# Performance work log

Hardware: AMD Instinct MI355X
Metric: run time of the kernel (lower is better)

Reference implementation:

```python
import jax, jax.numpy as jnp
import numpy as np

TAU = 0.07
MIN_PIXELS = 3
LAMBDA_CF = 0.5
NUM_INST = 16  # labels in patch_mask are 0 (bg) .. NUM_INST
N, D = 65536, 256


def _l2norm(x, axis=-1):
    n = jnp.linalg.norm(x, axis=axis, keepdims=True)
    return x / jnp.maximum(n, 1e-12)


def setup_inputs() -> dict:
    key = jax.random.key(0)
    k1, k2, k3 = jax.random.split(key, 3)
    dp = jax.random.normal(k1, (N, D), dtype=jnp.float32)
    f_cf = jax.random.normal(k2, (N, D), dtype=jnp.float32)
    patch_mask = jax.random.randint(k3, (N,), 0, NUM_INST + 1, dtype=jnp.int32)
    return {"dp": dp, "f_cf": f_cf, "patch_mask": patch_mask}


def reference(dp, f_cf, patch_mask):
    K1 = NUM_INST + 1  # segment 0 = background, 1..K = instances
    labels = patch_mask
    dpn = _l2norm(dp)       # [N, D]
    cfn = _l2norm(f_cf)     # [N, D]

    ones = jnp.ones((labels.shape[0],), dtype=dp.dtype)
    cnt = jax.ops.segment_sum(ones, labels, num_segments=K1)         # [K1]
    sum_dp = jax.ops.segment_sum(dpn, labels, num_segments=K1)       # [K1, D]
    sum_cf = jax.ops.segment_sum(cfn, labels, num_segments=K1)       # [K1, D]
    safe_cnt = jnp.maximum(cnt, 1.0)

    mu_dp = _l2norm(sum_dp / safe_cnt[:, None])   # per-segment normalized mean of dp
    mu_cf = _l2norm(sum_cf / safe_cnt[:, None])   # per-segment normalized mean of f_cf
    mu_bg_dp = mu_dp[0]                           # [D]
    mu_bg_cf = mu_cf[0]                           # [D]

    # per-pixel similarities
    pos_t = jnp.sum(dpn * mu_dp[labels], axis=-1)      # dp . mu_{k(label)}
    neg_t = dpn @ mu_bg_dp                             # dp . mu_bg
    # -log(exp(p/tau)/(exp(p/tau)+exp(n/tau))) == softplus((n-p)/tau)
    pix_loss_t = jax.nn.softplus((neg_t - pos_t) / TAU)

    pos_cf = cfn @ mu_bg_cf                            # f_cf . mu_bg_cf (the 'pos' in the cf term)
    oth_cf = jnp.sum(cfn * mu_cf[labels], axis=-1)     # f_cf . mu_k_cf
    pix_loss_cf = jax.nn.softplus((oth_cf - pos_cf) / TAU)

    seg_loss_t = jax.ops.segment_sum(pix_loss_t, labels, num_segments=K1) / safe_cnt
    seg_loss_cf = jax.ops.segment_sum(pix_loss_cf, labels, num_segments=K1) / safe_cnt

    inst_ids = jnp.arange(K1)
    valid = (inst_ids > 0) & (cnt >= MIN_PIXELS)       # instances with enough pixels
    n_valid = jnp.maximum(jnp.sum(valid.astype(dp.dtype)), 1.0)

    loss_t = jnp.sum(jnp.where(valid, seg_loss_t, 0.0)) / n_valid
    loss_cf = jnp.sum(jnp.where(valid, seg_loss_cf, 0.0)) / n_valid
    return loss_t + LAMBDA_CF * loss_cf
```

## Files before the change

kernel.cpp:

```cpp
#include <hip/hip_runtime.h>
#include <math.h>

#define K1 17
#define SEG_F (K1 * 256)
#define PART_F (2 * SEG_F + 32)
#define NGRP 8

#define SCALE_SUM 65536.0f
#define INV_SUM   (1.0f / 65536.0f)
#define SCALE_L   8192.0f
#define INV_L     (1.0f / 8192.0f)

#define GRED_BASE 0
#define MU_BASE   (NGRP * 2 * SEG_F)
#define GCNT_OFF  (MU_BASE + 2 * SEG_F)
#define LT_OFF    (GCNT_OFF + K1)
#define LC_OFF    (LT_OFF + K1)
#define PART_BASE 78400

template <int CTRL, int RMASK>
__device__ __forceinline__ float dpp_add(float x) {
    int t = __builtin_amdgcn_update_dpp(0, __float_as_int(x), CTRL, RMASK, 0xf, false);
    return x + __int_as_float(t);
}
__device__ __forceinline__ float wave_sum_nb(float x) {
    x = dpp_add<0x111, 0xf>(x);
    x = dpp_add<0x112, 0xf>(x);
    x = dpp_add<0x114, 0xf>(x);
    x = dpp_add<0x118, 0xf>(x);
    x = dpp_add<0x142, 0xa>(x);
    x = dpp_add<0x143, 0xc>(x);
    return x;
}
__device__ __forceinline__ float wave_sum(float x) {
    return __int_as_float(__builtin_amdgcn_readlane(__float_as_int(wave_sum_nb(x)), 63));
}
__device__ __forceinline__ float dot4s(const float4 v) {
    return v.x * v.x + v.y * v.y + v.z * v.z + v.w * v.w;
}
__device__ __forceinline__ float softplus_f(float x) {
    const float a = -fabsf(x) * 1.4426950408889634f;
    float e; asm("v_exp_f32 %0, %1" : "=v"(e) : "v"(a));
    float l; asm("v_log_f32 %0, %1" : "=v"(l) : "v"(1.0f + e));
    return fmaxf(x, 0.0f) + l * 0.6931471805599453f;
}
__device__ __forceinline__ float rsq_f(float x) {
    float r; asm("v_rsq_f32 %0, %1" : "=v"(r) : "v"(x));
    return r;
}

__device__ __forceinline__ void kA_commit(int* __restrict__ s, const float4 v, const float4 w,
                                          float nd, float nc, int l, int lane)
{
    const float f = SCALE_SUM * rsq_f(fmaxf(nd, 1e-24f));
    const float g = SCALE_SUM * rsq_f(fmaxf(nc, 1e-24f));
    int* a = s + l * 256 + lane;
    atomicAdd(a,       (int)(v.x * f));
    atomicAdd(a + 64,  (int)(v.y * f));
    atomicAdd(a + 128, (int)(v.z * f));
    atomicAdd(a + 192, (int)(v.w * f));
    int* b = a + SEG_F;
    atomicAdd(b,       (int)(w.x * g));
    atomicAdd(b + 64,  (int)(w.y * g));
    atomicAdd(b + 128, (int)(w.z * g));
    atomicAdd(b + 192, (int)(w.w * g));
}

__global__ __launch_bounds__(1024) void kA(const float4* __restrict__ dp, const float4* __restrict__ cf,
                                           const int* __restrict__ mask, float* __restrict__ part,
                                           int nPart, int nRows)
{
    __shared__ int s[2 * SEG_F];
    __shared__ int hist[K1];
    const int tid = threadIdx.x;
    for (int i = tid; i < 2 * SEG_F; i += 1024) s[i] = 0;
    if (tid < K1) hist[tid] = 0;
    __syncthreads();

    const int lane = tid & 63;
    const int wid = tid >> 6;
    const int rpb = (nRows + nPart - 1) / nPart;
    const int base = blockIdx.x * rpb;
    const int end = (base + rpb < nRows) ? base + rpb : nRows;

    int r = base + wid;
    for (; r + 16 < end; r += 32) {
        const int l0 = mask[r], l1 = mask[r + 16];
        const float4 v0 = dp[(size_t)r * 64 + lane];
        const float4 w0 = cf[(size_t)r * 64 + lane];
        const float4 v1 = dp[(size_t)(r + 16) * 64 + lane];
        const float4 w1 = cf[(size_t)(r + 16) * 64 + lane];
        const float nd0 = wave_sum(dot4s(v0));
        const float nc0 = wave_sum(dot4s(w0));
        const float nd1 = wave_sum(dot4s(v1));
        const float nc1 = wave_sum(dot4s(w1));
        kA_commit(s, v0, w0, nd0, nc0, l0, lane);
        kA_commit(s, v1, w1, nd1, nc1, l1, lane);
        if (lane == 0) { atomicAdd(&hist[l0], 1); atomicAdd(&hist[l1], 1); }
    }
    for (; r < end; r += 16) {
        const int l0 = mask[r];
        const float4 v0 = dp[(size_t)r * 64 + lane];
        const float4 w0 = cf[(size_t)r * 64 + lane];
        const float nd0 = wave_sum(dot4s(v0));
        const float nc0 = wave_sum(dot4s(w0));
        kA_commit(s, v0, w0, nd0, nc0, l0, lane);
        if (lane == 0) atomicAdd(&hist[l0], 1);
    }
    __syncthreads();
    float* outp = part + (size_t)blockIdx.x * PART_F;
    for (int i = tid; i < 2 * SEG_F; i += 1024) outp[i] = (float)s[i] * INV_SUM;
    if (tid < K1) outp[2 * SEG_F + tid] = (float)hist[tid];
}

__global__ __launch_bounds__(256) void kRed(const float* __restrict__ part, float* __restrict__ gred, int nPart)
{
    const int col = blockIdx.x * 256 + threadIdx.x;
    const int g = blockIdx.y;
    const int per = nPart / NGRP;
    const float* p = part + (size_t)g * per * PART_F + col;
    float acc = 0.0f;
    for (int b = 0; b < per; ++b) acc += p[(size_t)b * PART_F];
    gred[g * (2 * SEG_F) + col] = acc;
}

__global__ __launch_bounds__(256) void k_mu(float* __restrict__ ws, int nPart)
{
    const int k = blockIdx.x, t = threadIdx.x;
    __shared__ float C[256];
    float c = 0.0f;
    for (int b = t; b < nPart; b += 256) c += ws[PART_BASE + (size_t)b * PART_F + 2 * SEG_F + k];
    C[t] = c; __syncthreads();
    for (int s2 = 128; s2 > 0; s2 >>= 1) { if (t < s2) C[t] += C[t + s2]; __syncthreads(); }
    const float cnt = C[0];
    const float safe = fmaxf(cnt, 1.0f);
    float sd = 0.0f, sc = 0.0f;
    #pragma unroll
    for (int g = 0; g < NGRP; ++g) {
        sd += ws[GRED_BASE + g * 2 * SEG_F + k * 256 + t];
        sc += ws[GRED_BASE + g * 2 * SEG_F + SEG_F + k * 256 + t];
    }
    const float md = sd / safe, mc = sc / safe;
    __shared__ float A[256], B[256];
    A[t] = md * md; B[t] = mc * mc;
    __syncthreads();
    for (int s2 = 128; s2 > 0; s2 >>= 1) { if (t < s2) { A[t] += A[t + s2]; B[t] += B[t + s2]; } __syncthreads(); }
    const float id = 1.0f / fmaxf(sqrtf(A[0]), 1e-12f);
    const float ic = 1.0f / fmaxf(sqrtf(B[0]), 1e-12f);
    const int dnat = 4 * (t & 63) + (t >> 6);
    ws[MU_BASE + k * 256 + dnat]         = md * id;
    ws[MU_BASE + SEG_F + k * 256 + dnat] = mc * ic;
    if (t == 0) ws[GCNT_OFF + k] = cnt;
}

__device__ __forceinline__ void row_part(const float4 v, const float4 w, int l, int lane,
                                         const float4* __restrict__ mud, const float4* __restrict__ muc,
                                         const float4 bd, const float4 bc,
                                         float& nd, float& nc, float& dd, float& dc)
{
    const float4 md = mud[l * 64 + lane];
    const float4 mc = muc[l * 64 + lane];
    nd = dot4s(v);
    nc = dot4s(w);
    dd = v.x * (bd.x - md.x) + v.y * (bd.y - md.y) + v.z * (bd.z - md.z) + v.w * (bd.w - md.w);
    dc = w.x * (mc.x - bc.x) + w.y * (mc.y - bc.y) + w.z * (mc.z - bc.z) + w.w * (mc.w - bc.w);
}
__device__ __forceinline__ void row_commit(float nd, float nc, float dd, float dc, int l, int tid63,
                                           int* __restrict__ lt, int* __restrict__ lc)
{
    const float invd = rsq_f(fmaxf(nd, 1e-24f));
    const float invc = rsq_f(fmaxf(nc, 1e-24f));
    const float xt = dd * invd * (1.0f / 0.07f);
    const float xc = dc * invc * (1.0f / 0.07f);
    const float plt = softplus_f(xt);
    const float plc = softplus_f(xc);
    if (tid63) {
        atomicAdd(&lt[l], (int)(plt * SCALE_L + 0.5f));
        atomicAdd(&lc[l], (int)(plc * SCALE_L + 0.5f));
    }
}

__global__ __launch_bounds__(512) void k_loss(const float4* __restrict__ dp, const float4* __restrict__ cf,
                                              const int* __restrict__ mask, float* __restrict__ ws,
                                              int nBlocks, int nRows)
{
    __shared__ float4 mud[SEG_F / 4], muc[SEG_F / 4];
    __shared__ int lt[K1], lc[K1];
    const int tid = threadIdx.x;
    const float4* musrc = (const float4*)(ws + MU_BASE);
    for (int i = tid; i < SEG_F / 4; i += 512) { mud[i] = musrc[i]; muc[i] = musrc[SEG_F / 4 + i]; }
    if (tid < K1) { lt[tid] = 0; lc[tid] = 0; }
    __syncthreads();

    const int lane = tid & 63;
    const int wid = tid >> 6;
    const int rpb = (nRows + nBlocks - 1) / nBlocks;
    const int base = blockIdx.x * rpb;
    const int end = (base + rpb < nRows) ? base + rpb : nRows;
    const int isl63 = (lane == 63);

    const float4 bd = mud[lane];
    const float4 bc = muc[lane];

    int r = base + wid;
    for (; r + 8 < end; r += 16) {
        const int l0 = mask[r], l1 = mask[r + 8];
        const float4 v0 = dp[(size_t)r * 64 + lane];
        const float4 w0 = cf[(size_t)r * 64 + lane];
        const float4 v1 = dp[(size_t)(r + 8) * 64 + lane];
        const float4 w1 = cf[(size_t)(r + 8) * 64 + lane];
        float nd0, nc0, dd0, dc0, nd1, nc1, dd1, dc1;
        row_part(v0, w0, l0, lane, mud, muc, bd, bc, nd0, nc0, dd0, dc0);
        row_part(v1, w1, l1, lane, mud, muc, bd, bc, nd1, nc1, dd1, dc1);
        nd0 = wave_sum_nb(nd0); nc0 = wave_sum_nb(nc0); dd0 = wave_sum_nb(dd0); dc0 = wave_sum_nb(dc0);
        nd1 = wave_sum_nb(nd1); nc1 = wave_sum_nb(nc1); dd1 = wave_sum_nb(dd1); dc1 = wave_sum_nb(dc1);
        row_commit(nd0, nc0, dd0, dc0, l0, isl63, lt, lc);
        row_commit(nd1, nc1, dd1, dc1, l1, isl63, lt, lc);
    }
    for (; r < end; r += 8) {
        const int l0 = mask[r];
        const float4 v0 = dp[(size_t)r * 64 + lane];
        const float4 w0 = cf[(size_t)r * 64 + lane];
        float nd0, nc0, dd0, dc0;
        row_part(v0, w0, l0, lane, mud, muc, bd, bc, nd0, nc0, dd0, dc0);
        nd0 = wave_sum_nb(nd0); nc0 = wave_sum_nb(nc0); dd0 = wave_sum_nb(dd0); dc0 = wave_sum_nb(dc0);
        row_commit(nd0, nc0, dd0, dc0, l0, isl63, lt, lc);
    }
    __syncthreads();
    if (tid < K1) {
        int* LT = (int*)ws + LT_OFF;
        int* LC = (int*)ws + LC_OFF;
        atomicAdd(&LT[tid], lt[tid]);
        atomicAdd(&LC[tid], lc[tid]);
    }
}

__global__ void k_final(const float* __restrict__ ws, float* __restrict__ out)
{
    const int t = threadIdx.x;
    const int* LT = (const int*)ws + LT_OFF;
    const int* LC = (const int*)ws + LC_OFF;
    float vt = 0.0f, vc = 0.0f, nv = 0.0f;
    if (t >= 1 && t < K1) {
        const float cnt = ws[GCNT_OFF + t];
        if (cnt >= 3.0f) {
            const float safe = fmaxf(cnt, 1.0f);
            vt = (float)LT[t] * INV_L / safe;
            vc = (float)LC[t] * INV_L / safe;
            nv = 1.0f;
        }
    }
    #pragma unroll
    for (int o = 32; o > 0; o >>= 1) {
        vt += __shfl_xor(vt, o, 64);
        vc += __shfl_xor(vc, o, 64);
        nv += __shfl_xor(nv, o, 64);
    }
    if (t == 0) {
        const float n = fmaxf(nv, 1.0f);
        out[0] = vt / n + 0.5f * (vc / n);
    }
}

extern "C" void kernel_launch(void* const* d_in, const int* in_sizes, int n_in,
                              void* d_out, int out_size, void* d_ws, size_t ws_size,
                              hipStream_t stream)
{
    const float4* dp = (const float4*)d_in[0];
    const float4* cf = (const float4*)d_in[1];
    const int* mask  = (const int*)d_in[2];
    float* ws  = (float*)d_ws;
    float* out = (float*)d_out;
    const int nRows = in_sizes[2];

    long availF = (long)(ws_size / 4) - PART_BASE;
    int nPart = (int)(availF / PART_F);
    if (nPart > 512) nPart = 512;
    nPart &= ~7;
    if (nPart < 8) nPart = 8;

    hipMemsetAsync((void*)(ws + LT_OFF), 0, 2 * K1 * sizeof(int), stream);
    kA<<<nPart, 1024, 0, stream>>>(dp, cf, mask, ws + PART_BASE, nPart, nRows);
    kRed<<<dim3(34, NGRP), 256, 0, stream>>>(ws + PART_BASE, ws + GRED_BASE, nPart);
    k_mu<<<K1, 256, 0, stream>>>(ws, nPart);
    const int nB3 = 1024;
    k_loss<<<nB3, 512, 0, stream>>>(dp, cf, mask, ws, nB3, nRows);
    k_final<<<1, 64, 0, stream>>>(ws, out);
}
```

Before: 97.69 us.

## Fuse final reduction into loss kernel via last-block counter, drop memset launch

Removes the separate k_final launch by having the last k_loss block, detected through an atomic done counter, compute the final scalar. The accumulator zeroing moves from a hipMemsetAsync into k_mu, removing another launch. The partial-block count in kA is also capped at 256 instead of 512, which gives kA fewer, larger blocks and leaves kRed less to reduce. In exchange it adds threadfences and a serial tail in one thread, and relies on the memory ordering of the completion counter.

```diff
diff --git a/kernel.cpp b/kernel.cpp
--- a/kernel.cpp
+++ b/kernel.cpp
@@ -16,6 +16,7 @@
 #define GCNT_OFF  (MU_BASE + 2 * SEG_F)
 #define LT_OFF    (GCNT_OFF + K1)
 #define LC_OFF    (LT_OFF + K1)
+#define DONE_OFF  (LC_OFF + K1)
 #define PART_BASE 78400
 
 template <int CTRL, int RMASK>
@@ -127,6 +128,7 @@
 __global__ __launch_bounds__(256) void k_mu(float* __restrict__ ws, int nPart)
 {
     const int k = blockIdx.x, t = threadIdx.x;
+    if (k == 0 && t < 2 * K1 + 1) ((int*)ws)[LT_OFF + t] = 0;
     __shared__ float C[256];
     float c = 0.0f;
     for (int b = t; b < nPart; b += 256) c += ws[PART_BASE + (size_t)b * PART_F + 2 * SEG_F + k];
@@ -182,7 +184,7 @@
 
 __global__ __launch_bounds__(512) void k_loss(const float4* __restrict__ dp, const float4* __restrict__ cf,
                                               const int* __restrict__ mask, float* __restrict__ ws,
-                                              int nBlocks, int nRows)
+                                              float* __restrict__ out, int nBlocks, int nRows)
 {
     __shared__ float4 mud[SEG_F / 4], muc[SEG_F / 4];
     __shared__ int lt[K1], lc[K1];
@@ -227,38 +229,31 @@
         row_commit(nd0, nc0, dd0, dc0, l0, isl63, lt, lc);
     }
     __syncthreads();
+    int* LT = (int*)ws + LT_OFF;
+    int* LC = (int*)ws + LC_OFF;
     if (tid < K1) {
-        int* LT = (int*)ws + LT_OFF;
-        int* LC = (int*)ws + LC_OFF;
         atomicAdd(&LT[tid], lt[tid]);
         atomicAdd(&LC[tid], lc[tid]);
     }
-}
-
-__global__ void k_final(const float* __restrict__ ws, float* __restrict__ out)
-{
-    const int t = threadIdx.x;
-    const int* LT = (const int*)ws + LT_OFF;
-    const int* LC = (const int*)ws + LC_OFF;
-    float vt = 0.0f, vc = 0.0f, nv = 0.0f;
-    if (t >= 1 && t < K1) {
-        const float cnt = ws[GCNT_OFF + t];
-        if (cnt >= 3.0f) {
-            const float safe = fmaxf(cnt, 1.0f);
-            vt = (float)LT[t] * INV_L / safe;
-            vc = (float)LC[t] * INV_L / safe;
-            nv = 1.0f;
+    __syncthreads();
+    if (tid == 0) {
+        __threadfence();
+        const int prev = atomicAdd((int*)ws + DONE_OFF, 1);
+        if (prev == nBlocks - 1) {
+            __threadfence();
+            float vt = 0.0f, vc = 0.0f, nv = 0.0f;
+            for (int k = 1; k < K1; ++k) {
+                const float cnt = ws[GCNT_OFF + k];
+                if (cnt >= 3.0f) {
+                    const float safe = fmaxf(cnt, 1.0f);
+                    vt += (float)atomicAdd(&LT[k], 0) * INV_L / safe;
+                    vc += (float)atomicAdd(&LC[k], 0) * INV_L / safe;
+                    nv += 1.0f;
+                }
+            }
+            const float n = fmaxf(nv, 1.0f);
+            out[0] = vt / n + 0.5f * (vc / n);
         }
-    }
-    #pragma unroll
-    for (int o = 32; o > 0; o >>= 1) {
-        vt += __shfl_xor(vt, o, 64);
-        vc += __shfl_xor(vc, o, 64);
-        nv += __shfl_xor(nv, o, 64);
-    }
-    if (t == 0) {
-        const float n = fmaxf(nv, 1.0f);
-        out[0] = vt / n + 0.5f * (vc / n);
     }
 }
 
@@ -275,15 +270,13 @@
 
     long availF = (long)(ws_size / 4) - PART_BASE;
     int nPart = (int)(availF / PART_F);
-    if (nPart > 512) nPart = 512;
+    if (nPart > 256) nPart = 256;
     nPart &= ~7;
     if (nPart < 8) nPart = 8;
 
-    hipMemsetAsync((void*)(ws + LT_OFF), 0, 2 * K1 * sizeof(int), stream);
     kA<<<nPart, 1024, 0, stream>>>(dp, cf, mask, ws + PART_BASE, nPart, nRows);
     kRed<<<dim3(34, NGRP), 256, 0, stream>>>(ws + PART_BASE, ws + GRED_BASE, nPart);
     k_mu<<<K1, 256, 0, stream>>>(ws, nPart);
     const int nB3 = 1024;
-    k_loss<<<nB3, 512, 0, stream>>>(dp, cf, mask, ws, nB3, nRows);
-    k_final<<<1, 64, 0, stream>>>(ws, out);
-}
+    k_loss<<<nB3, 512, 0, stream>>>(dp, cf, mask, ws, out, nB3, nRows);
+}
```

New measurement: 99.81 us. 1.02x slower.

## Cache normalized rows as FP8 in pass one and fold mu differences

Applied to the files above, without the earlier changes.

The first pass now also writes each row's L2-normalized dp and f_cf vectors as scaled FP8 into the workspace. The loss pass then reads these 1-byte copies instead of re-reading both fp32 inputs, and no longer recomputes row norms. k_mu now precomputes the difference between the background and segment mean vectors, so the loss pass needs one dot product per tensor. The memset is folded into k_mu and the partition count is fixed. The aim is to cut the second pass's HBM traffic, at the cost of FP8 quantization error in the per-pixel dots, which the softplus amplifies through the 1/tau scale.

```diff
diff --git a/kernel.cpp b/kernel.cpp
--- a/kernel.cpp
+++ b/kernel.cpp
@@ -5,11 +5,14 @@
 #define SEG_F (K1 * 256)
 #define PART_F (2 * SEG_F + 32)
 #define NGRP 8
+#define NPART 256
 
 #define SCALE_SUM 65536.0f
 #define INV_SUM   (1.0f / 65536.0f)
 #define SCALE_L   8192.0f
 #define INV_L     (1.0f / 8192.0f)
+#define FP8_SCALE 16.0f
+#define TAU_INV   (1.0f / 0.07f)
 
 #define GRED_BASE 0
 #define MU_BASE   (NGRP * 2 * SEG_F)
@@ -17,6 +20,9 @@
 #define LT_OFF    (GCNT_OFF + K1)
 #define LC_OFF    (LT_OFF + K1)
 #define PART_BASE 78400
+#define FP8D_BASE (PART_BASE + NPART * PART_F)
+
+typedef float v2f __attribute__((ext_vector_type(2)));
 
 template <int CTRL, int RMASK>
 __device__ __forceinline__ float dpp_add(float x) {
@@ -49,11 +55,15 @@
     return r;
 }
 
+template <bool W8>
 __device__ __forceinline__ void kA_commit(int* __restrict__ s, const float4 v, const float4 w,
-                                          float nd, float nc, int l, int lane)
-{
-    const float f = SCALE_SUM * rsq_f(fmaxf(nd, 1e-24f));
-    const float g = SCALE_SUM * rsq_f(fmaxf(nc, 1e-24f));
+                                          float nd, float nc, int l, int lane,
+                                          unsigned* __restrict__ q8d, unsigned* __restrict__ q8c)
+{
+    const float ir = rsq_f(fmaxf(nd, 1e-24f));
+    const float jr = rsq_f(fmaxf(nc, 1e-24f));
+    const float f = SCALE_SUM * ir;
+    const float g = SCALE_SUM * jr;
     int* a = s + l * 256 + lane;
     atomicAdd(a,       (int)(v.x * f));
     atomicAdd(a + 64,  (int)(v.y * f));
@@ -64,10 +74,22 @@
     atomicAdd(b + 64,  (int)(w.y * g));
     atomicAdd(b + 128, (int)(w.z * g));
     atomicAdd(b + 192, (int)(w.w * g));
-}
-
+    if (W8) {
+        const float fe = FP8_SCALE * ir;
+        const float ge = FP8_SCALE * jr;
+        int pd = __builtin_amdgcn_cvt_pk_fp8_f32(v.x * fe, v.y * fe, 0, false);
+        pd     = __builtin_amdgcn_cvt_pk_fp8_f32(v.z * fe, v.w * fe, pd, true);
+        int pc = __builtin_amdgcn_cvt_pk_fp8_f32(w.x * ge, w.y * ge, 0, false);
+        pc     = __builtin_amdgcn_cvt_pk_fp8_f32(w.z * ge, w.w * ge, pc, true);
+        *q8d = (unsigned)pd;
+        *q8c = (unsigned)pc;
+    }
+}
+
+template <bool W8>
 __global__ __launch_bounds__(1024) void kA(const float4* __restrict__ dp, const float4* __restrict__ cf,
                                            const int* __restrict__ mask, float* __restrict__ part,
+                                           unsigned* __restrict__ qd, unsigned* __restrict__ qc,
                                            int nPart, int nRows)
 {
     __shared__ int s[2 * SEG_F];
@@ -94,8 +116,8 @@
         const float nc0 = wave_sum(dot4s(w0));
         const float nd1 = wave_sum(dot4s(v1));
         const float nc1 = wave_sum(dot4s(w1));
-        kA_commit(s, v0, w0, nd0, nc0, l0, lane);
-        kA_commit(s, v1, w1, nd1, nc1, l1, lane);
+        kA_commit<W8>(s, v0, w0, nd0, nc0, l0, lane, qd + (size_t)r * 64 + lane,        qc + (size_t)r * 64 + lane);
+        kA_commit<W8>(s, v1, w1, nd1, nc1, l1, lane, qd + (size_t)(r + 16) * 64 + lane, qc + (size_t)(r + 16) * 64 + lane);
         if (lane == 0) { atomicAdd(&hist[l0], 1); atomicAdd(&hist[l1], 1); }
     }
     for (; r < end; r += 16) {
@@ -104,7 +126,7 @@
         const float4 w0 = cf[(size_t)r * 64 + lane];
         const float nd0 = wave_sum(dot4s(v0));
         const float nc0 = wave_sum(dot4s(w0));
-        kA_commit(s, v0, w0, nd0, nc0, l0, lane);
+        kA_commit<W8>(s, v0, w0, nd0, nc0, l0, lane, qd + (size_t)r * 64 + lane, qc + (size_t)r * 64 + lane);
         if (lane == 0) atomicAdd(&hist[l0], 1);
     }
     __syncthreads();
@@ -127,68 +149,69 @@
 __global__ __launch_bounds__(256) void k_mu(float* __restrict__ ws, int nPart)
 {
     const int k = blockIdx.x, t = threadIdx.x;
+    if (k == 0 && t < 2 * K1) ((int*)ws)[LT_OFF + t] = 0;
     __shared__ float C[256];
     float c = 0.0f;
     for (int b = t; b < nPart; b += 256) c += ws[PART_BASE + (size_t)b * PART_F + 2 * SEG_F + k];
     C[t] = c; __syncthreads();
     for (int s2 = 128; s2 > 0; s2 >>= 1) { if (t < s2) C[t] += C[t + s2]; __syncthreads(); }
     const float cnt = C[0];
-    const float safe = fmaxf(cnt, 1.0f);
-    float sd = 0.0f, sc = 0.0f;
+    __syncthreads();
+    float c0 = 0.0f;
+    for (int b = t; b < nPart; b += 256) c0 += ws[PART_BASE + (size_t)b * PART_F + 2 * SEG_F];
+    C[t] = c0; __syncthreads();
+    for (int s2 = 128; s2 > 0; s2 >>= 1) { if (t < s2) C[t] += C[t + s2]; __syncthreads(); }
+    const float cnt0 = C[0];
+
+    const float safek = fmaxf(cnt, 1.0f), safe0 = fmaxf(cnt0, 1.0f);
+    float sdk = 0, sck = 0, sd0 = 0, sc0 = 0;
     #pragma unroll
     for (int g = 0; g < NGRP; ++g) {
-        sd += ws[GRED_BASE + g * 2 * SEG_F + k * 256 + t];
-        sc += ws[GRED_BASE + g * 2 * SEG_F + SEG_F + k * 256 + t];
-    }
-    const float md = sd / safe, mc = sc / safe;
+        const float* gr = ws + GRED_BASE + g * 2 * SEG_F;
+        sdk += gr[k * 256 + t];  sck += gr[SEG_F + k * 256 + t];
+        sd0 += gr[t];            sc0 += gr[SEG_F + t];
+    }
+    const float mdk = sdk / safek, mck = sck / safek;
+    const float md0 = sd0 / safe0, mc0 = sc0 / safe0;
     __shared__ float A[256], B[256];
-    A[t] = md * md; B[t] = mc * mc;
+    A[t] = mdk * mdk; B[t] = mck * mck;
     __syncthreads();
     for (int s2 = 128; s2 > 0; s2 >>= 1) { if (t < s2) { A[t] += A[t + s2]; B[t] += B[t + s2]; } __syncthreads(); }
-    const float id = 1.0f / fmaxf(sqrtf(A[0]), 1e-12f);
-    const float ic = 1.0f / fmaxf(sqrtf(B[0]), 1e-12f);
+    const float idk = 1.0f / fmaxf(sqrtf(A[0]), 1e-12f);
+    const float ick = 1.0f / fmaxf(sqrtf(B[0]), 1e-12f);
+    __syncthreads();
+    A[t] = md0 * md0; B[t] = mc0 * mc0;
+    __syncthreads();
+    for (int s2 = 128; s2 > 0; s2 >>= 1) { if (t < s2) { A[t] += A[t + s2]; B[t] += B[t + s2]; } __syncthreads(); }
+    const float id0 = 1.0f / fmaxf(sqrtf(A[0]), 1e-12f);
+    const float ic0 = 1.0f / fmaxf(sqrtf(B[0]), 1e-12f);
     const int dnat = 4 * (t & 63) + (t >> 6);
-    ws[MU_BASE + k * 256 + dnat]         = md * id;
-    ws[MU_BASE + SEG_F + k * 256 + dnat] = mc * ic;
+    ws[MU_BASE + k * 256 + dnat]         = md0 * id0 - mdk * idk;
+    ws[MU_BASE + SEG_F + k * 256 + dnat] = mck * ick - mc0 * ic0;
     if (t == 0) ws[GCNT_OFF + k] = cnt;
 }
 
-__device__ __forceinline__ void row_part(const float4 v, const float4 w, int l, int lane,
-                                         const float4* __restrict__ mud, const float4* __restrict__ muc,
-                                         const float4 bd, const float4 bc,
-                                         float& nd, float& nc, float& dd, float& dc)
-{
-    const float4 md = mud[l * 64 + lane];
-    const float4 mc = muc[l * 64 + lane];
-    nd = dot4s(v);
-    nc = dot4s(w);
-    dd = v.x * (bd.x - md.x) + v.y * (bd.y - md.y) + v.z * (bd.z - md.z) + v.w * (bd.w - md.w);
-    dc = w.x * (mc.x - bc.x) + w.y * (mc.y - bc.y) + w.z * (mc.z - bc.z) + w.w * (mc.w - bc.w);
-}
-__device__ __forceinline__ void row_commit(float nd, float nc, float dd, float dc, int l, int tid63,
-                                           int* __restrict__ lt, int* __restrict__ lc)
-{
-    const float invd = rsq_f(fmaxf(nd, 1e-24f));
-    const float invc = rsq_f(fmaxf(nc, 1e-24f));
-    const float xt = dd * invd * (1.0f / 0.07f);
-    const float xc = dc * invc * (1.0f / 0.07f);
+__device__ __forceinline__ void q_commit(float dd, float dc, int l, int isl63,
+                                         int* __restrict__ lt, int* __restrict__ lc)
+{
+    const float xt = dd * (TAU_INV / FP8_SCALE);
+    const float xc = dc * (TAU_INV / FP8_SCALE);
     const float plt = softplus_f(xt);
     const float plc = softplus_f(xc);
-    if (tid63) {
+    if (isl63) {
         atomicAdd(&lt[l], (int)(plt * SCALE_L + 0.5f));
         atomicAdd(&lc[l], (int)(plc * SCALE_L + 0.5f));
     }
 }
-
-__global__ __launch_bounds__(512) void k_loss(const float4* __restrict__ dp, const float4* __restrict__ cf,
-                                              const int* __restrict__ mask, float* __restrict__ ws,
-                                              int nBlocks, int nRows)
-{
-    __shared__ float4 mud[SEG_F / 4], muc[SEG_F / 4];
+__global__ __launch_bounds__(512) void k_loss8(const unsigned* __restrict__ qd, const unsigned* __restrict__ qc,
+                                               const int* __restrict__ mask, float* __restrict__ ws,
+                                               int nBlocks, int nRows)
+{
+    __shared__ float4 dmud[SEG_F / 4], dmuc[SEG_F / 4];
     __shared__ int lt[K1], lc[K1];
     const int tid = threadIdx.x;
     const float4* musrc = (const float4*)(ws + MU_BASE);
-    for (int i = tid; i < SEG_F / 4; i += 512) { mud[i] = musrc[i]; muc[i] = musrc[SEG_F / 4 + i]; }
+    for (int i = tid; i < SEG_F / 4; i += 512) { dmud[i] = musrc[i]; dmuc[i] = musrc[SEG_F / 4 + i]; }
     if (tid < K1) { lt[tid] = 0; lc[tid] = 0; }
     __syncthreads();
 
@@ -199,39 +222,86 @@
     const int end = (base + rpb < nRows) ? base + rpb : nRows;
     const int isl63 = (lane == 63);
 
-    const float4 bd = mud[lane];
-    const float4 bc = muc[lane];
-
     int r = base + wid;
     for (; r + 8 < end; r += 16) {
         const int l0 = mask[r], l1 = mask[r + 8];
-        const float4 v0 = dp[(size_t)r * 64 + lane];
-        const float4 w0 = cf[(size_t)r * 64 + lane];
-        const float4 v1 = dp[(size_t)(r + 8) * 64 + lane];
-        const float4 w1 = cf[(size_t)(r + 8) * 64 + lane];
-        float nd0, nc0, dd0, dc0, nd1, nc1, dd1, dc1;
-        row_part(v0, w0, l0, lane, mud, muc, bd, bc, nd0, nc0, dd0, dc0);
-        row_part(v1, w1, l1, lane, mud, muc, bd, bc, nd1, nc1, dd1, dc1);
-        nd0 = wave_sum_nb(nd0); nc0 = wave_sum_nb(nc0); dd0 = wave_sum_nb(dd0); dc0 = wave_sum_nb(dc0);
-        nd1 = wave_sum_nb(nd1); nc1 = wave_sum_nb(nc1); dd1 = wave_sum_nb(dd1); dc1 = wave_sum_nb(dc1);
-        row_commit(nd0, nc0, dd0, dc0, l0, isl63, lt, lc);
-        row_commit(nd1, nc1, dd1, dc1, l1, isl63, lt, lc);
+        const unsigned a0 = qd[(size_t)r * 64 + lane],       b0 = qc[(size_t)r * 64 + lane];
+        const unsigned a1 = qd[(size_t)(r + 8) * 64 + lane], b1 = qc[(size_t)(r + 8) * 64 + lane];
+        const float4 D0 = dmud[l0 * 64 + lane], C0 = dmuc[l0 * 64 + lane];
+        const float4 D1 = dmud[l1 * 64 + lane], C1 = dmuc[l1 * 64 + lane];
+        const v2f al0 = __builtin_amdgcn_cvt_pk_f32_fp8((int)a0, false), ah0 = __builtin_amdgcn_cvt_pk_f32_fp8((int)a0, true);
+        const v2f bl0 = __builtin_amdgcn_cvt_pk_f32_fp8((int)b0, false), bh0 = __builtin_amdgcn_cvt_pk_f32_fp8((int)b0, true);
+        const v2f al1 = __builtin_amdgcn_cvt_pk_f32_fp8((int)a1, false), ah1 = __builtin_amdgcn_cvt_pk_f32_fp8((int)a1, true);
+        const v2f bl1 = __builtin_amdgcn_cvt_pk_f32_fp8((int)b1, false), bh1 = __builtin_amdgcn_cvt_pk_f32_fp8((int)b1, true);
+        float dd0 = al0.x * D0.x + al0.y * D0.y + ah0.x * D0.z + ah0.y * D0.w;
+        float dc0 = bl0.x * C0.x + bl0.y * C0.y + bh0.x * C0.z + bh0.y * C0.w;
+        float dd1 = al1.x * D1.x + al1.y * D1.y + ah1.x * D1.z + ah1.y * D1.w;
+        float dc1 = bl1.x * C1.x + bl1.y * C1.y + bh1.x * C1.z + bh1.y * C1.w;
+        dd0 = wave_sum_nb(dd0); dc0 = wave_sum_nb(dc0);
+        dd1 = wave_sum_nb(dd1); dc1 = wave_sum_nb(dc1);
+        q_commit(dd0, dc0, l0, isl63, lt, lc);
+        q_commit(dd1, dc1, l1, isl63, lt, lc);
     }
     for (; r < end; r += 8) {
+        const int l0 = mask[r];
+        const unsigned a0 = qd[(size_t)r * 64 + lane], b0 = qc[(size_t)r * 64 + lane];
+        const float4 D0 = dmud[l0 * 64 + lane], C0 = dmuc[l0 * 64 + lane];
+        const v2f al0 = __builtin_amdgcn_cvt_pk_f32_fp8((int)a0, false), ah0 = __builtin_amdgcn_cvt_pk_f32_fp8((int)a0, true);
+        const v2f bl0 = __builtin_amdgcn_cvt_pk_f32_fp8((int)b0, false), bh0 = __builtin_amdgcn_cvt_pk_f32_fp8((int)b0, true);
+        float dd0 = al0.x * D0.x + al0.y * D0.y + ah0.x * D0.z + ah0.y * D0.w;
+        float dc0 = bl0.x * C0.x + bl0.y * C0.y + bh0.x * C0.z + bh0.y * C0.w;
+        dd0 = wave_sum_nb(dd0); dc0 = wave_sum_nb(dc0);
+        q_commit(dd0, dc0, l0, isl63, lt, lc);
+    }
+    __syncthreads();
+    if (tid < K1) {
+        atomicAdd((int*)ws + LT_OFF + tid, lt[tid]);
+        atomicAdd((int*)ws + LC_OFF + tid, lc[tid]);
+    }
+}
+
+__global__ __launch_bounds__(512) void k_lossraw(const float4* __restrict__ dp, const float4* __restrict__ cf,
+                                                 const int* __restrict__ mask, float* __restrict__ ws,
+                                                 int nBlocks, int nRows)
+{
+    __shared__ float4 dmud[SEG_F / 4], dmuc[SEG_F / 4];
+    __shared__ int lt[K1], lc[K1];
+    const int tid = threadIdx.x;
+    const float4* musrc = (const float4*)(ws + MU_BASE);
+    for (int i = tid; i < SEG_F / 4; i += 512) { dmud[i] = musrc[i]; dmuc[i] = musrc[SEG_F / 4 + i]; }
+    if (tid < K1) { lt[tid] = 0; lc[tid] = 0; }
+    __syncthreads();
+
+    const int lane = tid & 63;
+    const int wid = tid >> 6;
+    const int rpb = (nRows + nBlocks - 1) / nBlocks;
+    const int base = blockIdx.x * rpb;
+    const int end = (base + rpb < nRows) ? base + rpb : nRows;
+    const int isl63 = (lane == 63);
+
+    for (int r = base + wid; r < end; r += 8) {
         const int l0 = mask[r];
         const float4 v0 = dp[(size_t)r * 64 + lane];
         const float4 w0 = cf[(size_t)r * 64 + lane];
-        float nd0, nc0, dd0, dc0;
-        row_part(v0, w0, l0, lane, mud, muc, bd, bc, nd0, nc0, dd0, dc0);
-        nd0 = wave_sum_nb(nd0); nc0 = wave_sum_nb(nc0); dd0 = wave_sum_nb(dd0); dc0 = wave_sum_nb(dc0);
-        row_commit(nd0, nc0, dd0, dc0, l0, isl63, lt, lc);
+        const float4 D0 = dmud[l0 * 64 + lane], C0 = dmuc[l0 * 64 + lane];
+        float nd = dot4s(v0), nc = dot4s(w0);
+        float dd = v0.x * D0.x + v0.y * D0.y + v0.z * D0.z + v0.w * D0.w;
+        float dc = w0.x * C0.x + w0.y * C0.y + w0.z * C0.z + w0.w * C0.w;
+        nd = wave_sum_nb(nd); nc = wave_sum_nb(nc);
+        dd = wave_sum_nb(dd); dc = wave_sum_nb(dc);
+        const float xt = dd * rsq_f(fmaxf(nd, 1e-24f)) * TAU_INV;
+        const float xc = dc * rsq_f(fmaxf(nc, 1e-24f)) * TAU_INV;
+        const float plt = softplus_f(xt);
+        const float plc = softplus_f(xc);
+        if (isl63) {
+            atomicAdd(&lt[l0], (int)(plt * SCALE_L + 0.5f));
+            atomicAdd(&lc[l0], (int)(plc * SCALE_L + 0.5f));
+        }
     }
     __syncthreads();
     if (tid < K1) {
-        int* LT = (int*)ws + LT_OFF;
-        int* LC = (int*)ws + LC_OFF;
-        atomicAdd(&LT[tid], lt[tid]);
-        atomicAdd(&LC[tid], lc[tid]);
+        atomicAdd((int*)ws + LT_OFF + tid, lt[tid]);
+        atomicAdd((int*)ws + LC_OFF + tid, lc[tid]);
     }
 }
 
@@ -273,17 +343,20 @@
     float* out = (float*)d_out;
     const int nRows = in_sizes[2];
 
-    long availF = (long)(ws_size / 4) - PART_BASE;
-    int nPart = (int)(availF / PART_F);
-    if (nPart > 512) nPart = 512;
-    nPart &= ~7;
-    if (nPart < 8) nPart = 8;
-
-    hipMemsetAsync((void*)(ws + LT_OFF), 0, 2 * K1 * sizeof(int), stream);
-    kA<<<nPart, 1024, 0, stream>>>(dp, cf, mask, ws + PART_BASE, nPart, nRows);
-    kRed<<<dim3(34, NGRP), 256, 0, stream>>>(ws + PART_BASE, ws + GRED_BASE, nPart);
-    k_mu<<<K1, 256, 0, stream>>>(ws, nPart);
+    unsigned* qd = (unsigned*)ws + FP8D_BASE;
+    unsigned* qc = qd + (size_t)nRows * 64;
+    const bool use8 = (ws_size / 4) >= (size_t)FP8D_BASE + 2 * (size_t)nRows * 64;
+
+    if (use8)
+        kA<true><<<NPART, 1024, 0, stream>>>(dp, cf, mask, ws + PART_BASE, qd, qc, NPART, nRows);
+    else
+        kA<false><<<NPART, 1024, 0, stream>>>(dp, cf, mask, ws + PART_BASE, qd, qc, NPART, nRows);
+    kRed<<<dim3(34, NGRP), 256, 0, stream>>>(ws + PART_BASE, ws + GRED_BASE, NPART);
+    k_mu<<<K1, 256, 0, stream>>>(ws, NPART);
     const int nB3 = 1024;
-    k_loss<<<nB3, 512, 0, stream>>>(dp, cf, mask, ws, nB3, nRows);
+    if (use8)
+        k_loss8<<<nB3, 512, 0, stream>>>(qd, qc, mask, ws, nB3, nRows);
+    else
+        k_lossraw<<<nB3, 512, 0, stream>>>(dp, cf, mask, ws, nB3, nRows);
     k_final<<<1, 64, 0, stream>>>(ws, out);
 }
```

Measured after the change: 80.79 us. 17.3% less time.
